# Kernel tuning notes

Hardware: AMD Instinct MI355X
Metric: run time of the kernel (lower is better)

## Reference

```python
import jax, jax.numpy as jnp
import numpy as np

H, HKV, D = 32, 8, 128          # query heads, kv heads, head dim
G = H // HKV                     # GQA group size
PAGE, TOPK = 64, 64              # page size, top-k pages per (b, kv-head)
SCALE = D ** -0.5


def rotate_half(x):
    x1, x2 = x[..., : x.shape[-1] // 2], x[..., x.shape[-1] // 2 :]
    return jnp.concatenate((-x2, x1), axis=-1)


def setup_inputs() -> dict:
    key = jax.random.key(0)
    ks = jax.random.split(key, 8)
    B, Q, HID, S = 4, 1, 4096, 16384
    hidden_states = jax.random.normal(ks[0], (B, Q, HID), jnp.float32)
    # rotary embedding for current decode position S
    inv_freq = 1.0 / (10000.0 ** (np.arange(0, D, 2, dtype=np.float32) / D))
    ang = np.float32(S) * inv_freq
    emb = np.concatenate([ang, ang])  # [D]
    cos = jnp.broadcast_to(jnp.asarray(np.cos(emb))[None, None, :], (B, Q, D)).astype(jnp.float32)
    sin = jnp.broadcast_to(jnp.asarray(np.sin(emb))[None, None, :], (B, Q, D)).astype(jnp.float32)
    k_cache = jax.random.normal(ks[1], (B, HKV, S, D), jnp.float32)
    v_cache = jax.random.normal(ks[2], (B, HKV, S, D), jnp.float32)
    Wq = jax.random.normal(ks[3], (H * D, HID), jnp.float32) * 0.02
    Wk = jax.random.normal(ks[4], (HKV * D, HID), jnp.float32) * 0.02
    Wv = jax.random.normal(ks[5], (HKV * D, HID), jnp.float32) * 0.02
    Wo = jax.random.normal(ks[6], (HID, H * D), jnp.float32) * 0.02
    return dict(hidden_states=hidden_states, cos=cos, sin=sin,
                k_cache=k_cache, v_cache=v_cache, Wq=Wq, Wk=Wk, Wv=Wv, Wo=Wo)


def reference(hidden_states, cos, sin, k_cache, v_cache, Wq, Wk, Wv, Wo):
    B, Q, HID = hidden_states.shape
    S = k_cache.shape[2]
    P = S // PAGE

    # QKV projections (Linear, no bias) -> [B, heads, Q, D]
    q = (hidden_states @ Wq.T).reshape(B, Q, H, D).transpose(0, 2, 1, 3)
    k_new = (hidden_states @ Wk.T).reshape(B, Q, HKV, D).transpose(0, 2, 1, 3)
    v_new = (hidden_states @ Wv.T).reshape(B, Q, HKV, D).transpose(0, 2, 1, 3)

    # RoPE (unsqueeze_dim=1)
    c, s = cos[:, None, :, :], sin[:, None, :, :]
    q = q * c + rotate_half(q) * s
    k_new = k_new * c + rotate_half(k_new) * s

    # merge grouped query heads to kv heads (reduce='mean', merge_mode='kv')
    q_merged = q.reshape(B, HKV, G, Q, D).mean(axis=2)[:, :, 0, :]  # [B, HKV, D]

    # Quest page summaries: per-page elementwise min/max of keys
    Kp = k_cache.reshape(B, HKV, P, PAGE, D)
    Vp = v_cache.reshape(B, HKV, P, PAGE, D)
    kmin = Kp.min(axis=3)  # [B, HKV, P, D]
    kmax = Kp.max(axis=3)
    qm = q_merged[:, :, None, :]
    page_scores = jnp.maximum(qm * kmin, qm * kmax).sum(axis=-1)  # [B, HKV, P]

    # top-k page selection per (batch, kv head), gather selected pages
    _, idx = jax.lax.top_k(page_scores, TOPK)  # [B, HKV, TOPK]
    gidx = idx[:, :, :, None, None]
    K_sel = jnp.take_along_axis(Kp, gidx, axis=2).reshape(B, HKV, TOPK * PAGE, D)
    V_sel = jnp.take_along_axis(Vp, gidx, axis=2).reshape(B, HKV, TOPK * PAGE, D)

    # append current decode token's kv
    K = jnp.concatenate([K_sel, k_new], axis=2)  # [B, HKV, L, D]
    V = jnp.concatenate([V_sel, v_new], axis=2)

    # GQA attention over gathered sparse KV (no mask in quest decode path)
    qg = q.reshape(B, HKV, G, Q, D)
    logits = jnp.einsum('bhgqd,bhld->bhgql', qg, K) * SCALE
    w = jax.nn.softmax(logits.astype(jnp.float32), axis=-1).astype(q.dtype)
    o = jnp.einsum('bhgql,bhld->bhgqd', w, V)              # [B, HKV, G, Q, D]
    o = o.reshape(B, H, Q, D).transpose(0, 2, 1, 3).reshape(B, Q, H * D)
    return o @ Wo.T  # [B, Q, HID]
```

## Files before the change

kernel.cpp:

```cpp
#include <hip/hip_runtime.h>
#include <hip/hip_bf16.h>
#include <math.h>

constexpr int NB    = 4;
constexpr int NHID  = 4096;
constexpr int NHEAD = 32;
constexpr int NKV   = 8;
constexpr int NGQ   = 4;
constexpr int ND    = 128;
constexpr int NS    = 16384;
constexpr int NPG   = 64;
constexpr int NP    = 256;
constexpr int NTOP  = 64;
constexpr int NSPLIT = 32;
constexpr float FSCALE = 0.08838834764831845f;

__global__ __launch_bounds__(256) void k_qkv(
    const float* __restrict__ hs, const float* __restrict__ Wq,
    const float* __restrict__ Wk, const float* __restrict__ Wv,
    float* __restrict__ qkv) {
  int row0 = blockIdx.x * 4;
  int t = threadIdx.x;
  const float4* x4 = (const float4*)hs;
  const float4* wr[4];
#pragma unroll
  for (int r = 0; r < 4; r++) {
    int row = row0 + r;
    const float* w;
    if (row < 4096)      w = Wq + (size_t)row * NHID;
    else if (row < 5120) w = Wk + (size_t)(row - 4096) * NHID;
    else                 w = Wv + (size_t)(row - 5120) * NHID;
    wr[r] = (const float4*)w;
  }
  float acc[4][4] = {};
  for (int j = t; j < NHID / 4; j += 256) {
    float4 x0 = x4[j], x1 = x4[1024 + j], x2 = x4[2048 + j], x3 = x4[3072 + j];
#pragma unroll
    for (int r = 0; r < 4; r++) {
      float4 w4 = wr[r][j];
      acc[r][0] += w4.x * x0.x + w4.y * x0.y + w4.z * x0.z + w4.w * x0.w;
      acc[r][1] += w4.x * x1.x + w4.y * x1.y + w4.z * x1.z + w4.w * x1.w;
      acc[r][2] += w4.x * x2.x + w4.y * x2.y + w4.z * x2.z + w4.w * x2.w;
      acc[r][3] += w4.x * x3.x + w4.y * x3.y + w4.z * x3.z + w4.w * x3.w;
    }
  }
  __shared__ float red[4][16];
  int lane = t & 63, wv = t >> 6;
#pragma unroll
  for (int r = 0; r < 4; r++)
#pragma unroll
    for (int b = 0; b < 4; b++) {
      float v = acc[r][b];
      v += __shfl_down(v, 32); v += __shfl_down(v, 16); v += __shfl_down(v, 8);
      v += __shfl_down(v, 4);  v += __shfl_down(v, 2);  v += __shfl_down(v, 1);
      if (lane == 0) red[wv][r * 4 + b] = v;
    }
  __syncthreads();
  if (t < 16) {
    int r = t >> 2, b = t & 3;
    float s = red[0][t] + red[1][t] + red[2][t] + red[3][t];
    qkv[(size_t)b * 6144 + row0 + r] = s;
  }
}

__global__ __launch_bounds__(256) void k_pagescore(
    const float* __restrict__ kc, const float* __restrict__ qkv,
    const float* __restrict__ cosp, const float* __restrict__ sinp,
    float* __restrict__ scores) {
  int bid = blockIdx.x;
  int p = bid & (NP - 1);
  int bh = bid >> 8;
  int b = bh >> 3, kv = bh & 7;
  int t = threadIdx.x;
  __shared__ float sq[4][ND];
  __shared__ __align__(16) float qmS[ND];
  {
    int g = t >> 6, i = t & 63;
    int h = kv * NGQ + g;
    const float* cs = cosp + b * ND;
    const float* sn = sinp + b * ND;
    const float* q = qkv + (size_t)b * 6144 + h * ND;
    float x1 = q[i], x2 = q[i + 64];
    sq[g][i]      = x1 * cs[i] - x2 * sn[i];
    sq[g][i + 64] = x2 * cs[i + 64] + x1 * sn[i + 64];
  }
  __syncthreads();
  if (t < 128) {
    qmS[t] = 0.25f * (sq[0][t] + sq[1][t] + sq[2][t] + sq[3][t]);
  }
  const float4* Kp = (const float4*)(kc + ((size_t)bh * NS + (size_t)p * NPG) * ND);
  int c4 = t & 31, rg = t >> 5;
  float4 mn = make_float4(INFINITY, INFINITY, INFINITY, INFINITY);
  float4 mx = make_float4(-INFINITY, -INFINITY, -INFINITY, -INFINITY);
#pragma unroll
  for (int r = 0; r < 8; r++) {
    float4 v = Kp[(rg * 8 + r) * 32 + c4];
    mn.x = fminf(mn.x, v.x); mn.y = fminf(mn.y, v.y);
    mn.z = fminf(mn.z, v.z); mn.w = fminf(mn.w, v.w);
    mx.x = fmaxf(mx.x, v.x); mx.y = fmaxf(mx.y, v.y);
    mx.z = fmaxf(mx.z, v.z); mx.w = fmaxf(mx.w, v.w);
  }
  __shared__ float4 smn[8][32], smx[8][32];
  smn[rg][c4] = mn; smx[rg][c4] = mx;
  __syncthreads();
  if (t < 32) {
    float4 a = smn[0][t], b4 = smx[0][t];
#pragma unroll
    for (int r = 1; r < 8; r++) {
      float4 u = smn[r][t], w = smx[r][t];
      a.x = fminf(a.x, u.x); a.y = fminf(a.y, u.y);
      a.z = fminf(a.z, u.z); a.w = fminf(a.w, u.w);
      b4.x = fmaxf(b4.x, w.x); b4.y = fmaxf(b4.y, w.y);
      b4.z = fmaxf(b4.z, w.z); b4.w = fmaxf(b4.w, w.w);
    }
    const float4 qv = ((const float4*)qmS)[t];
    float s = fmaxf(qv.x * a.x, qv.x * b4.x)
            + fmaxf(qv.y * a.y, qv.y * b4.y)
            + fmaxf(qv.z * a.z, qv.z * b4.z)
            + fmaxf(qv.w * a.w, qv.w * b4.w);
    s += __shfl_xor(s, 1); s += __shfl_xor(s, 2); s += __shfl_xor(s, 4);
    s += __shfl_xor(s, 8); s += __shfl_xor(s, 16);
    if (t == 0) scores[bid] = s;
  }
}

__global__ __launch_bounds__(256) void k_attn_part(
    const float* __restrict__ kc, const float* __restrict__ vc,
    const float* __restrict__ qkv, const float* __restrict__ cosp,
    const float* __restrict__ sinp, const float* __restrict__ scores,
    float* __restrict__ part_l, float* __restrict__ part_o) {
  int idx = blockIdx.x;
  int sp = idx & (NSPLIT - 1);
  int bh = idx / NSPLIT;
  int b = bh >> 3, kv = bh & 7;
  int t = threadIdx.x;
  int g = t >> 6, lane = t & 63;
  int h = kv * NGQ + g;
  int half = lane >> 5;
  int li = lane & 31;
  __shared__ float s_sc[NP];
  __shared__ int s_pg[2];
  if (t < NP) s_sc[t] = scores[(size_t)bh * NP + t];
  __syncthreads();
  {
    float mine = s_sc[t];
    int rank = 0;
    for (int j = 0; j < NP; j++) {
      float v = s_sc[j];
      rank += (v > mine) || (v == mine && j < t);
    }
    if (rank == sp * 2)     s_pg[0] = t;
    if (rank == sp * 2 + 1) s_pg[1] = t;
  }
  float4 qv;
  {
    const float4* q4 = (const float4*)(qkv + (size_t)b * 6144 + h * ND);
    const float4* c4p = (const float4*)(cosp + b * ND);
    const float4* s4p = (const float4*)(sinp + b * ND);
    float4 qa = q4[li], qp = q4[li ^ 16];
    float4 cc = c4p[li], ss = s4p[li];
    float sgn = (li < 16) ? -1.f : 1.f;
    qv.x = qa.x * cc.x + sgn * qp.x * ss.x;
    qv.y = qa.y * cc.y + sgn * qp.y * ss.y;
    qv.z = qa.z * cc.z + sgn * qp.z * ss.z;
    qv.w = qa.w * cc.w + sgn * qp.w * ss.w;
  }
  __syncthreads();
  int page0 = s_pg[0], page1 = s_pg[1];
  const float4* K0 = (const float4*)(kc + ((size_t)bh * NS + (size_t)page0 * NPG) * ND);
  const float4* V0 = (const float4*)(vc + ((size_t)bh * NS + (size_t)page0 * NPG) * ND);
  const float4* K1 = (const float4*)(kc + ((size_t)bh * NS + (size_t)page1 * NPG) * ND);
  const float4* V1 = (const float4*)(vc + ((size_t)bh * NS + (size_t)page1 * NPG) * ND);
  float lsum = 0.f;
  float4 o = make_float4(0.f, 0.f, 0.f, 0.f);
  for (int r2 = 0; r2 < NPG / 2; r2++) {
    int r = r2 * 2 + half;
    float4 ka = K0[r * 32 + li];
    float4 kb = K1[r * 32 + li];
    float d0 = ka.x * qv.x + ka.y * qv.y + ka.z * qv.z + ka.w * qv.w;
    float d1 = kb.x * qv.x + kb.y * qv.y + kb.z * qv.z + kb.w * qv.w;
    d0 += __shfl_xor(d0, 1);  d1 += __shfl_xor(d1, 1);
    d0 += __shfl_xor(d0, 2);  d1 += __shfl_xor(d1, 2);
    d0 += __shfl_xor(d0, 4);  d1 += __shfl_xor(d1, 4);
    d0 += __shfl_xor(d0, 8);  d1 += __shfl_xor(d1, 8);
    d0 += __shfl_xor(d0, 16); d1 += __shfl_xor(d1, 16);
    float w0 = __expf(d0 * FSCALE);
    float w1 = __expf(d1 * FSCALE);
    lsum += w0 + w1;
    float4 va = V0[r * 32 + li];
    float4 vb = V1[r * 32 + li];
    o.x += w0 * va.x + w1 * vb.x;
    o.y += w0 * va.y + w1 * vb.y;
    o.z += w0 * va.z + w1 * vb.z;
    o.w += w0 * va.w + w1 * vb.w;
  }
  o.x += __shfl_xor(o.x, 32); o.y += __shfl_xor(o.y, 32);
  o.z += __shfl_xor(o.z, 32); o.w += __shfl_xor(o.w, 32);
  lsum += __shfl_xor(lsum, 32);
  if (half == 0) {
    float4* po = (float4*)(part_o + (((size_t)bh * NGQ + g) * NSPLIT + sp) * ND);
    po[li] = o;
    if (li == 0) part_l[((size_t)bh * NGQ + g) * NSPLIT + sp] = lsum;
  }
}

__global__ __launch_bounds__(64) void k_combine(
    const float* __restrict__ qkv, const float* __restrict__ cosp,
    const float* __restrict__ sinp, const float* __restrict__ part_l,
    const float* __restrict__ part_o, float* __restrict__ attno) {
  int bid = blockIdx.x;
  int b = bid >> 5, h = bid & 31;
  int kv = h >> 2, g = h & 3;
  int lane = threadIdx.x;
  int bh = b * NKV + kv;
  const float2* c2p = (const float2*)(cosp + b * ND);
  const float2* s2p = (const float2*)(sinp + b * ND);
  float2 cc = c2p[lane], ss = s2p[lane];
  float sgn = (lane < 32) ? -1.f : 1.f;
  const float2* q2 = (const float2*)(qkv + (size_t)b * 6144 + h * ND);
  float2 qa = q2[lane], qp = q2[lane ^ 32];
  float2 qv;
  qv.x = qa.x * cc.x + sgn * qp.x * ss.x;
  qv.y = qa.y * cc.y + sgn * qp.y * ss.y;
  const float2* k2 = (const float2*)(qkv + (size_t)b * 6144 + 4096 + kv * ND);
  float2 ka = k2[lane], kp = k2[lane ^ 32];
  float2 kk;
  kk.x = ka.x * cc.x + sgn * kp.x * ss.x;
  kk.y = ka.y * cc.y + sgn * kp.y * ss.y;
  float d = qv.x * kk.x + qv.y * kk.y;
  d += __shfl_xor(d, 1); d += __shfl_xor(d, 2); d += __shfl_xor(d, 4);
  d += __shfl_xor(d, 8); d += __shfl_xor(d, 16); d += __shfl_xor(d, 32);
  float wn = __expf(d * FSCALE);
  const float2* v2 = (const float2*)(qkv + (size_t)b * 6144 + 5120 + kv * ND);
  float2 vv = v2[lane];
  float ox = wn * vv.x, oy = wn * vv.y, lt = wn;
  const float* pl = part_l + ((size_t)bh * NGQ + g) * NSPLIT;
  const float2* po = (const float2*)(part_o + (((size_t)bh * NGQ + g) * NSPLIT) * ND);
  for (int s = 0; s < NSPLIT; s++) {
    lt += pl[s];
    float2 p = po[(size_t)s * 64 + lane];
    ox += p.x; oy += p.y;
  }
  float inv = 1.0f / lt;
  float2* ao = (float2*)(attno + ((size_t)b * NHEAD + h) * ND);
  ao[lane] = make_float2(ox * inv, oy * inv);
}

__global__ __launch_bounds__(256) void k_oproj(
    const float* __restrict__ Wo, const float* __restrict__ x,
    float* __restrict__ out) {
  int row0 = blockIdx.x * 4;
  int t = threadIdx.x;
  const float4* x4 = (const float4*)x;
  float acc[4][4] = {};
  for (int j = t; j < NHID / 4; j += 256) {
    float4 x0 = x4[j], x1 = x4[1024 + j], x2 = x4[2048 + j], x3 = x4[3072 + j];
#pragma unroll
    for (int r = 0; r < 4; r++) {
      float4 w4 = ((const float4*)(Wo + (size_t)(row0 + r) * NHID))[j];
      acc[r][0] += w4.x * x0.x + w4.y * x0.y + w4.z * x0.z + w4.w * x0.w;
      acc[r][1] += w4.x * x1.x + w4.y * x1.y + w4.z * x1.z + w4.w * x1.w;
      acc[r][2] += w4.x * x2.x + w4.y * x2.y + w4.z * x2.z + w4.w * x2.w;
      acc[r][3] += w4.x * x3.x + w4.y * x3.y + w4.z * x3.z + w4.w * x3.w;
    }
  }
  __shared__ float red[4][16];
  int lane = t & 63, wv = t >> 6;
#pragma unroll
  for (int r = 0; r < 4; r++)
#pragma unroll
    for (int b = 0; b < 4; b++) {
      float v = acc[r][b];
      v += __shfl_down(v, 32); v += __shfl_down(v, 16); v += __shfl_down(v, 8);
      v += __shfl_down(v, 4);  v += __shfl_down(v, 2);  v += __shfl_down(v, 1);
      if (lane == 0) red[wv][r * 4 + b] = v;
    }
  __syncthreads();
  if (t < 16) {
    int r = t >> 2, b = t & 3;
    float s = red[0][t] + red[1][t] + red[2][t] + red[3][t];
    out[(size_t)b * NHID + row0 + r] = s;
  }
}

extern "C" void kernel_launch(void* const* d_in, const int* in_sizes, int n_in,
                              void* d_out, int out_size, void* d_ws, size_t ws_size,
                              hipStream_t stream) {
  const float* hs   = (const float*)d_in[0];
  const float* cosp = (const float*)d_in[1];
  const float* sinp = (const float*)d_in[2];
  const float* kc   = (const float*)d_in[3];
  const float* vc   = (const float*)d_in[4];
  const float* Wq   = (const float*)d_in[5];
  const float* Wk   = (const float*)d_in[6];
  const float* Wv   = (const float*)d_in[7];
  const float* Wo   = (const float*)d_in[8];
  float* out = (float*)d_out;

  float* ws = (float*)d_ws;
  float* qkv    = ws;
  float* scores = ws + 24576;
  float* part_l = ws + 32768;
  float* part_o = ws + 36864;
  float* attno  = ws + 561152;

  k_qkv<<<6144 / 4, 256, 0, stream>>>(hs, Wq, Wk, Wv, qkv);
  k_pagescore<<<NB * NKV * NP, 256, 0, stream>>>(kc, qkv, cosp, sinp, scores);
  k_attn_part<<<NB * NKV * NSPLIT, 256, 0, stream>>>(kc, vc, qkv, cosp, sinp, scores, part_l, part_o);
  k_combine<<<NB * NHEAD, 64, 0, stream>>>(qkv, cosp, sinp, part_l, part_o, attno);
  k_oproj<<<NHID / 4, 256, 0, stream>>>(Wo, attno, out);
}
```

Baseline: 127.2 us.

## Score each page with one wavefront instead of a full block

The page-score kernel now gives each 64-lane wavefront its own page, so one block covers four pages and the grid is four times smaller. Each lane rebuilds its slice of the RoPE'd, group-averaged query in registers from float4 loads, replacing the shared-memory staging and barriers. Min/max over the page's rows is reduced with a cross-half shuffle instead of a shared-memory tree. The aim is to cut synchronisation and launch overhead and keep more independent K loads in flight per thread on this bandwidth-bound scan, at the cost of every wave recomputing the merged query.

```diff
diff --git a/kernel.cpp b/kernel.cpp
--- a/kernel.cpp
+++ b/kernel.cpp
@@ -67,61 +67,59 @@
     const float* __restrict__ kc, const float* __restrict__ qkv,
     const float* __restrict__ cosp, const float* __restrict__ sinp,
     float* __restrict__ scores) {
-  int bid = blockIdx.x;
-  int p = bid & (NP - 1);
-  int bh = bid >> 8;
+  int t = threadIdx.x;
+  int w = t >> 6, lane = t & 63;
+  int pid = blockIdx.x * 4 + w;
+  int bh = pid >> 8;
   int b = bh >> 3, kv = bh & 7;
-  int t = threadIdx.x;
-  __shared__ float sq[4][ND];
-  __shared__ __align__(16) float qmS[ND];
+  int c4 = lane & 31;
+  int r0 = lane >> 5;
+  float4 qm4 = make_float4(0.f, 0.f, 0.f, 0.f);
   {
-    int g = t >> 6, i = t & 63;
-    int h = kv * NGQ + g;
-    const float* cs = cosp + b * ND;
-    const float* sn = sinp + b * ND;
-    const float* q = qkv + (size_t)b * 6144 + h * ND;
-    float x1 = q[i], x2 = q[i + 64];
-    sq[g][i]      = x1 * cs[i] - x2 * sn[i];
-    sq[g][i + 64] = x2 * cs[i + 64] + x1 * sn[i + 64];
-  }
-  __syncthreads();
-  if (t < 128) {
-    qmS[t] = 0.25f * (sq[0][t] + sq[1][t] + sq[2][t] + sq[3][t]);
-  }
-  const float4* Kp = (const float4*)(kc + ((size_t)bh * NS + (size_t)p * NPG) * ND);
-  int c4 = t & 31, rg = t >> 5;
+    const float4* c4p = (const float4*)(cosp + b * ND);
+    const float4* s4p = (const float4*)(sinp + b * ND);
+    float4 cc = c4p[c4], ss = s4p[c4];
+    float sgn = (c4 < 16) ? -1.f : 1.f;
+#pragma unroll
+    for (int g = 0; g < 4; g++) {
+      const float4* q4 = (const float4*)(qkv + (size_t)b * 6144 + (kv * NGQ + g) * ND);
+      float4 qa = q4[c4], qp = q4[c4 ^ 16];
+      qm4.x += qa.x * cc.x + sgn * qp.x * ss.x;
+      qm4.y += qa.y * cc.y + sgn * qp.y * ss.y;
+      qm4.z += qa.z * cc.z + sgn * qp.z * ss.z;
+      qm4.w += qa.w * cc.w + sgn * qp.w * ss.w;
+    }
+    qm4.x *= 0.25f; qm4.y *= 0.25f; qm4.z *= 0.25f; qm4.w *= 0.25f;
+  }
+  const float4* Kp = (const float4*)(kc + (size_t)pid * NPG * ND);
   float4 mn = make_float4(INFINITY, INFINITY, INFINITY, INFINITY);
   float4 mx = make_float4(-INFINITY, -INFINITY, -INFINITY, -INFINITY);
 #pragma unroll
-  for (int r = 0; r < 8; r++) {
-    float4 v = Kp[(rg * 8 + r) * 32 + c4];
-    mn.x = fminf(mn.x, v.x); mn.y = fminf(mn.y, v.y);
-    mn.z = fminf(mn.z, v.z); mn.w = fminf(mn.w, v.w);
-    mx.x = fmaxf(mx.x, v.x); mx.y = fmaxf(mx.y, v.y);
-    mx.z = fmaxf(mx.z, v.z); mx.w = fmaxf(mx.w, v.w);
-  }
-  __shared__ float4 smn[8][32], smx[8][32];
-  smn[rg][c4] = mn; smx[rg][c4] = mx;
-  __syncthreads();
-  if (t < 32) {
-    float4 a = smn[0][t], b4 = smx[0][t];
-#pragma unroll
-    for (int r = 1; r < 8; r++) {
-      float4 u = smn[r][t], w = smx[r][t];
-      a.x = fminf(a.x, u.x); a.y = fminf(a.y, u.y);
-      a.z = fminf(a.z, u.z); a.w = fminf(a.w, u.w);
-      b4.x = fmaxf(b4.x, w.x); b4.y = fmaxf(b4.y, w.y);
-      b4.z = fmaxf(b4.z, w.z); b4.w = fmaxf(b4.w, w.w);
-    }
-    const float4 qv = ((const float4*)qmS)[t];
-    float s = fmaxf(qv.x * a.x, qv.x * b4.x)
-            + fmaxf(qv.y * a.y, qv.y * b4.y)
-            + fmaxf(qv.z * a.z, qv.z * b4.z)
-            + fmaxf(qv.w * a.w, qv.w * b4.w);
-    s += __shfl_xor(s, 1); s += __shfl_xor(s, 2); s += __shfl_xor(s, 4);
-    s += __shfl_xor(s, 8); s += __shfl_xor(s, 16);
-    if (t == 0) scores[bid] = s;
-  }
+  for (int rr = 0; rr < 4; rr++) {
+#pragma unroll
+    for (int j = 0; j < 8; j++) {
+      float4 v = Kp[((rr * 8 + j) * 2 + r0) * 32 + c4];
+      mn.x = fminf(mn.x, v.x); mn.y = fminf(mn.y, v.y);
+      mn.z = fminf(mn.z, v.z); mn.w = fminf(mn.w, v.w);
+      mx.x = fmaxf(mx.x, v.x); mx.y = fmaxf(mx.y, v.y);
+      mx.z = fmaxf(mx.z, v.z); mx.w = fmaxf(mx.w, v.w);
+    }
+  }
+  mn.x = fminf(mn.x, __shfl_xor(mn.x, 32));
+  mn.y = fminf(mn.y, __shfl_xor(mn.y, 32));
+  mn.z = fminf(mn.z, __shfl_xor(mn.z, 32));
+  mn.w = fminf(mn.w, __shfl_xor(mn.w, 32));
+  mx.x = fmaxf(mx.x, __shfl_xor(mx.x, 32));
+  mx.y = fmaxf(mx.y, __shfl_xor(mx.y, 32));
+  mx.z = fmaxf(mx.z, __shfl_xor(mx.z, 32));
+  mx.w = fmaxf(mx.w, __shfl_xor(mx.w, 32));
+  float s = fmaxf(qm4.x * mn.x, qm4.x * mx.x)
+          + fmaxf(qm4.y * mn.y, qm4.y * mx.y)
+          + fmaxf(qm4.z * mn.z, qm4.z * mx.z)
+          + fmaxf(qm4.w * mn.w, qm4.w * mx.w);
+  s += __shfl_xor(s, 1); s += __shfl_xor(s, 2); s += __shfl_xor(s, 4);
+  s += __shfl_xor(s, 8); s += __shfl_xor(s, 16);
+  if (lane == 0) scores[pid] = s;
 }
 
 __global__ __launch_bounds__(256) void k_attn_part(
@@ -305,7 +303,7 @@
   float* attno  = ws + 561152;
 
   k_qkv<<<6144 / 4, 256, 0, stream>>>(hs, Wq, Wk, Wv, qkv);
-  k_pagescore<<<NB * NKV * NP, 256, 0, stream>>>(kc, qkv, cosp, sinp, scores);
+  k_pagescore<<<NB * NKV * NP / 4, 256, 0, stream>>>(kc, qkv, cosp, sinp, scores);
   k_attn_part<<<NB * NKV * NSPLIT, 256, 0, stream>>>(kc, vc, qkv, cosp, sinp, scores, part_l, part_o);
   k_combine<<<NB * NHEAD, 64, 0, stream>>>(qkv, cosp, sinp, part_l, part_o, attno);
   k_oproj<<<NHID / 4, 256, 0, stream>>>(Wo, attno, out);
```

Result: no change. 127.9 us (+0.6%).
